# Kernel optimization log

Measured on AMD Instinct MI355X. Metric: run time of the kernel, lower is better.

## Reference

```python
import jax, jax.numpy as jnp
import numpy as np

D_MODEL = 1024
B, S = 4, 4096


def setup_inputs() -> dict:
    key = jax.random.key(0)
    k1, k2, k3, k4, k5 = jax.random.split(key, 5)
    lim = 1.0 / np.sqrt(D_MODEL)  # nn.Linear default init range
    x = jax.random.normal(k1, (B, S, D_MODEL), dtype=jnp.float32)
    mask = jnp.ones((B, S), dtype=jnp.float32)
    W_up = jax.random.uniform(k2, (D_MODEL, D_MODEL), jnp.float32, -lim, lim)
    b_up = jax.random.uniform(k3, (D_MODEL,), jnp.float32, -lim, lim)
    W_f = jax.random.uniform(k4, (D_MODEL, D_MODEL), jnp.float32, -lim, lim)
    b_f = jax.random.uniform(k5, (D_MODEL,), jnp.float32, -lim, lim)
    decay_param = jnp.zeros((1,), dtype=jnp.float32)
    return {"x": x, "mask": mask, "W_up": W_up, "b_up": b_up,
            "W_f": W_f, "b_f": b_f, "decay_param": decay_param}


def _decay_scan(u, decay):
    # h_t = decay * h_{t-1} + u_t  along axis=1, via associative scan.
    # Element: (a, b) representing h -> a*h + b; compose: (a1*a2, b1*a2 + b2).
    a = jnp.broadcast_to(decay, u.shape)

    def combine(c1, c2):
        a1, b1 = c1
        a2, b2 = c2
        return a1 * a2, b1 * a2 + b2

    _, h = jax.lax.associative_scan(combine, (a, u), axis=1)
    return h


def reference(x, mask, W_up, b_up, W_f, b_f, decay_param):
    decay = jax.nn.sigmoid(decay_param)[0]
    # u_i = mask_i * linear_update(x_i)
    u = (jnp.einsum('bsd,ed->bse', x, W_up) + b_up) * mask[..., None]
    # h_t = sum_{i<=t} decay^(t-i) * u_i  (exponential-decay recurrence)
    h = _decay_scan(u, decay)
    return jnp.einsum('bsd,ed->bse', h, W_f) + b_f
```

## Files before the change

kernel.cpp:

```cpp
#include <hip/hip_runtime.h>
#include <hip/hip_bf16.h>
#include <cstdint>
#include <cstddef>

#define DMODEL 1024
#define BATCH  4
#define SEQ    4096
#define BSROWS (BATCH*SEQ)
#define CHUNK  32
#define NCHUNK (SEQ/CHUNK)
#define NCH_T  (BATCH*NCHUNK)

typedef __attribute__((ext_vector_type(8))) short bf16x8;
typedef __attribute__((ext_vector_type(4))) float f32x4;


__device__ __forceinline__ unsigned short f2bf(float f) {
  union { float f; uint32_t u; } v; v.f = f;
  uint32_t u = v.u;
  u += 0x7FFFu + ((u >> 16) & 1u);
  return (unsigned short)(u >> 16);
}

__device__ __forceinline__ float sigmoid_dev(const float* dp) {
  return 1.0f / (1.0f + expf(-dp[0]));
}

typedef __attribute__((address_space(1))) void void_g;
typedef __attribute__((address_space(3))) void void_l;

__device__ __forceinline__ void gl2lds16(const void* g, void* l) {
  __builtin_amdgcn_global_load_lds((void_g*)g, (void_l*)l, 16, 0, 0);
}

__device__ __forceinline__ void kloop64(
    const unsigned short* __restrict__ A, const unsigned short* __restrict__ B,
    int m0, int n0, f32x4 acc[2][2],
    unsigned short* As, unsigned short* Bs, int tid) {
  int lane = tid & 63, w = tid >> 6, wm = w & 1, wn = w >> 1;
  int quad = lane >> 4, l16 = lane & 15;
  int r = tid >> 3, cch = tid & 7;
  int g = cch ^ (r & 7);
  const bf16x8* Av = (const bf16x8*)As;
  const bf16x8* Bv = (const bf16x8*)Bs;
  for (int k0 = 0; k0 < DMODEL; k0 += 64) {
    gl2lds16(A + (size_t)(m0 + r) * DMODEL + k0 + g * 8,      As + r * 64 + cch * 8);
    gl2lds16(A + (size_t)(m0 + 32 + r) * DMODEL + k0 + g * 8, As + (32 + r) * 64 + cch * 8);
    gl2lds16(B + (size_t)(n0 + r) * DMODEL + k0 + g * 8,      Bs + r * 64 + cch * 8);
    gl2lds16(B + (size_t)(n0 + 32 + r) * DMODEL + k0 + g * 8, Bs + (32 + r) * 64 + cch * 8);
    __syncthreads();
    #pragma unroll
    for (int kk = 0; kk < 2; ++kk) {
      bf16x8 af[2], bfr[2];
      #pragma unroll
      for (int i = 0; i < 2; ++i) {
        int rowA = wm * 32 + i * 16 + l16;
        af[i]  = Av[rowA * 8 + ((kk * 4 + quad) ^ (l16 & 7))];
        int rowB = wn * 32 + i * 16 + l16;
        bfr[i] = Bv[rowB * 8 + ((kk * 4 + quad) ^ (l16 & 7))];
      }
      #pragma unroll
      for (int i = 0; i < 2; ++i)
        #pragma unroll
        for (int j = 0; j < 2; ++j)
          acc[i][j] = __builtin_amdgcn_mfma_f32_16x16x32_bf16(af[i], bfr[j], acc[i][j], 0, 0, 0);
    }
    __syncthreads();
  }
}

__global__ __launch_bounds__(256) void prep_kernel(
    const float* __restrict__ x, const float* __restrict__ mask,
    const float* __restrict__ W_up, const float* __restrict__ b_up,
    const float* __restrict__ W_f, const float* __restrict__ dp,
    unsigned short* __restrict__ Wf_bf, unsigned short* __restrict__ WupT,
    float* __restrict__ bb, unsigned short* __restrict__ hv,
    float* __restrict__ carry, float* __restrict__ lbeta,
    float* __restrict__ cbeta) {
  __shared__ float tile[32][33];
  int blk = blockIdx.x;
  int tid = threadIdx.x;

  if (blk < 512) {
    float decay = sigmoid_dev(dp);
    int b = blk / NCHUNK, c = blk % NCHUNK;
    int base = b * SEQ + c * CHUNK;
    const float4* xp = (const float4*)(x + (size_t)base * DMODEL);
    const float4* mp4 = (const float4*)(mask + base);
    float mreg[32];
    #pragma unroll
    for (int q = 0; q < 8; ++q) {
      float4 t = mp4[q];
      mreg[q * 4 + 0] = t.x; mreg[q * 4 + 1] = t.y;
      mreg[q * 4 + 2] = t.z; mreg[q * 4 + 3] = t.w;
    }
    float4 h = make_float4(0.f, 0.f, 0.f, 0.f);
    #pragma unroll
    for (int s = 0; s < CHUNK; ++s) {
      float m = mreg[s];
      float4 xv = xp[(size_t)s * (DMODEL / 4) + tid];
      h.x = decay * h.x + m * xv.x;
      h.y = decay * h.y + m * xv.y;
      h.z = decay * h.z + m * xv.z;
      h.w = decay * h.w + m * xv.w;
      ushort4 o;
      o.x = f2bf(h.x); o.y = f2bf(h.y); o.z = f2bf(h.z); o.w = f2bf(h.w);
      ((ushort4*)hv)[(size_t)(base + s) * (DMODEL / 4) + tid] = o;
    }
    ((float4*)carry)[(size_t)blk * (DMODEL / 4) + tid] = h;
  } else if (blk < 1536) {
    int e = blk - 512;
    int lane = tid & 63, w = tid >> 6;
    float4 v = ((const float4*)(W_f + (size_t)e * DMODEL))[tid];
    float4 bu = ((const float4*)b_up)[tid];
    ushort4 o;
    o.x = f2bf(v.x); o.y = f2bf(v.y); o.z = f2bf(v.z); o.w = f2bf(v.w);
    ((ushort4*)(Wf_bf + (size_t)e * DMODEL))[tid] = o;
    float s = v.x * bu.x + v.y * bu.y + v.z * bu.z + v.w * bu.w;
    #pragma unroll
    for (int off = 32; off; off >>= 1) s += __shfl_down(s, off);
    if (lane == 0) ((float*)tile)[w] = s;
    __syncthreads();
    if (tid == 0)
      bb[e] = ((float*)tile)[0] + ((float*)tile)[1] +
              ((float*)tile)[2] + ((float*)tile)[3];
  } else if (blk < 2560) {
    int id = blk - 1536;
    int bx = id & 31, by = id >> 5;
    int tx = tid & 31, ty = tid >> 5;
    int xx = bx * 32 + tx;
    int y0 = by * 32;
    for (int j = ty; j < 32; j += 8)
      tile[j][tx] = W_up[(size_t)(y0 + j) * DMODEL + xx];
    __syncthreads();
    int ox = by * 32 + tx;
    int oy0 = bx * 32;
    for (int j = ty; j < 32; j += 8)
      WupT[(size_t)(oy0 + j) * DMODEL + ox] = f2bf(tile[tx][j]);
  } else {
    float decay = sigmoid_dev(dp);
    int t = (blk - 2560) * 256 + tid;
    int s = t & 31;
    int cbase = t & ~31;
    float hb = 0.f;
    for (int i = 0; i <= s; ++i)
      hb = decay * hb + mask[cbase + i];
    lbeta[t] = hb;
    if (s == 31) cbeta[t >> 5] = hb;
  }
}

__global__ __launch_bounds__(256) void mid2_kernel(
    const unsigned short* __restrict__ Wf_bf,
    const unsigned short* __restrict__ WupT,
    unsigned short* __restrict__ Wc,
    const float* __restrict__ carry, const float* __restrict__ cbeta,
    const float* __restrict__ dp,
    unsigned short* __restrict__ Pbf, float* __restrict__ pbeta) {
  __shared__ unsigned short As[64 * 64];
  __shared__ unsigned short Bs[64 * 64];
  int tid = threadIdx.x;
  if (blockIdx.x < 256) {
    int mt = blockIdx.x >> 4, nt = blockIdx.x & 15;
    f32x4 acc[2][2] = {};
    kloop64(Wf_bf, WupT, mt * 64, nt * 64, acc, As, Bs, tid);
    int lane = tid & 63, w = tid >> 6, wm = w & 1, wn = w >> 1;
    int quad = lane >> 4, l16 = lane & 15;
    #pragma unroll
    for (int j = 0; j < 2; ++j) {
      int col = nt * 64 + wn * 32 + j * 16 + l16;
      #pragma unroll
      for (int i = 0; i < 2; ++i) {
        int rowb = mt * 64 + wm * 32 + i * 16 + quad * 4;
        #pragma unroll
        for (int rr = 0; rr < 4; ++rr)
          Wc[(size_t)(rowb + rr) * DMODEL + col] = f2bf(acc[i][j][rr]);
      }
    }
  } else {
    float decay = sigmoid_dev(dp);
    float dL = powf(decay, (float)CHUNK);
    int gid = (blockIdx.x - 256) * 256 + tid;
    int b = gid >> 10, dd = gid & 1023;
    float P = 0.f;
    for (int c0 = 0; c0 < NCHUNK; c0 += 8) {
      float v[8];
      #pragma unroll
      for (int j = 0; j < 8; ++j)
        v[j] = carry[(size_t)(b * NCHUNK + c0 + j) * DMODEL + dd];
      #pragma unroll
      for (int j = 0; j < 8; ++j) {
        Pbf[(size_t)(b * NCHUNK + c0 + j) * DMODEL + dd] = f2bf(P);
        P = dL * P + v[j];
      }
    }
    if (dd == 0) {
      float Pb = 0.f;
      for (int c0 = 0; c0 < NCHUNK; c0 += 16) {
        float v[16];
        #pragma unroll
        for (int j = 0; j < 16; ++j) v[j] = cbeta[b * NCHUNK + c0 + j];
        #pragma unroll
        for (int j = 0; j < 16; ++j) {
          pbeta[b * NCHUNK + c0 + j] = Pb;
          Pb = dL * Pb + v[j];
        }
      }
    }
  }
}

__global__ __launch_bounds__(256) void pout_kernel(
    const unsigned short* __restrict__ Pbf,
    const unsigned short* __restrict__ Wc,
    const float* __restrict__ pbeta, const float* __restrict__ bb,
    float* __restrict__ Pout) {
  __shared__ unsigned short As[64 * 64];
  __shared__ unsigned short Bs[64 * 64];
  int tid = threadIdx.x;
  int mt = blockIdx.x >> 4, nt = blockIdx.x & 15;
  f32x4 acc[2][2] = {};
  kloop64(Pbf, Wc, mt * 64, nt * 64, acc, As, Bs, tid);
  int lane = tid & 63, w = tid >> 6, wm = w & 1, wn = w >> 1;
  int quad = lane >> 4, l16 = lane & 15;
  #pragma unroll
  for (int j = 0; j < 2; ++j) {
    int col = nt * 64 + wn * 32 + j * 16 + l16;
    float bbv = bb[col];
    #pragma unroll
    for (int i = 0; i < 2; ++i) {
      int rowb = mt * 64 + wm * 32 + i * 16 + quad * 4;
      #pragma unroll
      for (int rr = 0; rr < 4; ++rr) {
        int row = rowb + rr;
        Pout[(size_t)row * DMODEL + col] = acc[i][j][rr] + pbeta[row] * bbv;
      }
    }
  }
}

__global__ __launch_bounds__(256) void gemm_main(
    const unsigned short* __restrict__ A,
    const unsigned short* __restrict__ Bm,
    const float* __restrict__ Pout,
    const float* __restrict__ lbeta,
    const float* __restrict__ bb,
    const float* __restrict__ bias_f,
    const float* __restrict__ dp,
    float* __restrict__ out) {
  __shared__ unsigned short As[128 * 32];
  __shared__ unsigned short Bs[128 * 32];
  __shared__ float dpow[CHUNK];
  int tid = threadIdx.x;
  if (tid < CHUNK) {
    float decay = sigmoid_dev(dp);
    dpow[tid] = powf(decay, (float)(tid + 1));
  }
  int lane = tid & 63, w = tid >> 6, wm = w & 1, wn = w >> 1;
  int quad = lane >> 4, l16 = lane & 15;
  int r = tid >> 2;
  int c4 = tid & 3;
  int g = c4 ^ ((r >> 1) & 3);
  int phi = (l16 >> 1) & 3;
  int m0 = (blockIdx.x & 127) * 128;
  int n0 = (blockIdx.x >> 7) * 128;
  f32x4 acc[4][4] = {};
  const bf16x8* Av = (const bf16x8*)As;
  const bf16x8* Bv = (const bf16x8*)Bs;
  for (int k0 = 0; k0 < DMODEL; k0 += 32) {
    gl2lds16(A + (size_t)(m0 + r) * DMODEL + k0 + g * 8,        As + r * 32 + c4 * 8);
    gl2lds16(A + (size_t)(m0 + 64 + r) * DMODEL + k0 + g * 8,   As + (64 + r) * 32 + c4 * 8);
    gl2lds16(Bm + (size_t)(n0 + r) * DMODEL + k0 + g * 8,       Bs + r * 32 + c4 * 8);
    gl2lds16(Bm + (size_t)(n0 + 64 + r) * DMODEL + k0 + g * 8,  Bs + (64 + r) * 32 + c4 * 8);
    __syncthreads();
    bf16x8 af[4], bfr[4];
    #pragma unroll
    for (int i = 0; i < 4; ++i) {
      int rowA = wm * 64 + i * 16 + l16;
      af[i]  = Av[rowA * 4 + (quad ^ phi)];
      int rowB = wn * 64 + i * 16 + l16;
      bfr[i] = Bv[rowB * 4 + (quad ^ phi)];
    }
    #pragma unroll
    for (int i = 0; i < 4; ++i)
      #pragma unroll
      for (int j = 0; j < 4; ++j)
        acc[i][j] = __builtin_amdgcn_mfma_f32_16x16x32_bf16(af[i], bfr[j], acc[i][j], 0, 0, 0);
    __syncthreads();
  }
  #pragma unroll
  for (int j = 0; j < 4; ++j) {
    int col = n0 + wn * 64 + j * 16 + l16;
    float bbv = bb[col];
    float bfv = bias_f[col];
    #pragma unroll
    for (int i = 0; i < 4; ++i) {
      int rowb = m0 + wm * 64 + i * 16 + quad * 4;
      #pragma unroll
      for (int rr = 0; rr < 4; ++rr) {
        int row = rowb + rr;
        float po = Pout[(size_t)(row >> 5) * DMODEL + col];
        out[(size_t)row * DMODEL + col] =
            acc[i][j][rr] + dpow[row & 31] * po + lbeta[row] * bbv + bfv;
      }
    }
  }
}


extern "C" void kernel_launch(void* const* d_in, const int* in_sizes, int n_in,
                              void* d_out, int out_size, void* d_ws, size_t ws_size,
                              hipStream_t stream) {
  const float* x    = (const float*)d_in[0];
  const float* mask = (const float*)d_in[1];
  const float* W_up = (const float*)d_in[2];
  const float* b_up = (const float*)d_in[3];
  const float* W_f  = (const float*)d_in[4];
  const float* b_f  = (const float*)d_in[5];
  const float* dp   = (const float*)d_in[6];
  float* out = (float*)d_out;

  char* ws = (char*)d_ws;
  unsigned short* hv    = (unsigned short*)(ws);
  unsigned short* Wc    = (unsigned short*)(ws + 33554432);
  unsigned short* Wf_bf = (unsigned short*)(ws + 35651584);
  unsigned short* WupT  = (unsigned short*)(ws + 37748736);
  float* carry  = (float*)(ws + 39845888);
  unsigned short* Pbf = (unsigned short*)(ws + 41943040);
  float* Pout   = (float*)(ws + 42991616);
  float* lbeta  = (float*)(ws + 45088768);
  float* cbeta  = (float*)(ws + 45154304);
  float* pbeta  = (float*)(ws + 45156352);
  float* bb     = (float*)(ws + 45158400);

  prep_kernel<<<2624, 256, 0, stream>>>(x, mask, W_up, b_up, W_f, dp,
                                        Wf_bf, WupT, bb, hv, carry, lbeta, cbeta);
  mid2_kernel<<<272, 256, 0, stream>>>(Wf_bf, WupT, Wc, carry, cbeta, dp,
                                       Pbf, pbeta);
  pout_kernel<<<128, 256, 0, stream>>>(Pbf, Wc, pbeta, bb, Pout);
  gemm_main<<<1024, 256, 0, stream>>>(hv, Wc, Pout, lbeta, bb, b_f, dp, out);
}
```

Measured before the change: 203.8 us.

## Triple-buffer LDS tiles with async prefetch in all GEMM k-loops

Replaces the single-buffered load/sync/compute loop in kloop64 and gemm_main with a three-slot LDS ring. Each step issues global-to-LDS loads two tiles ahead, waits with vmcnt, and uses one barrier per step. MFMA sections are wrapped in s_setprio, and the gemm_main epilogue is reordered to hoist per-row loads. The goal is to overlap global memory latency with MFMA work, at the cost of three times the LDS footprint, which may lower occupancy.

Result: no change. 201.2 us (-1.3%).

```diff
diff --git a/kernel.cpp b/kernel.cpp
--- a/kernel.cpp
+++ b/kernel.cpp
@@ -41,14 +41,19 @@
   int quad = lane >> 4, l16 = lane & 15;
   int r = tid >> 3, cch = tid & 7;
   int g = cch ^ (r & 7);
-  const bf16x8* Av = (const bf16x8*)As;
-  const bf16x8* Bv = (const bf16x8*)Bs;
-  for (int k0 = 0; k0 < DMODEL; k0 += 64) {
-    gl2lds16(A + (size_t)(m0 + r) * DMODEL + k0 + g * 8,      As + r * 64 + cch * 8);
-    gl2lds16(A + (size_t)(m0 + 32 + r) * DMODEL + k0 + g * 8, As + (32 + r) * 64 + cch * 8);
-    gl2lds16(B + (size_t)(n0 + r) * DMODEL + k0 + g * 8,      Bs + r * 64 + cch * 8);
-    gl2lds16(B + (size_t)(n0 + 32 + r) * DMODEL + k0 + g * 8, Bs + (32 + r) * 64 + cch * 8);
-    __syncthreads();
+
+  auto stage = [&](int t, int slot) {
+    int k0 = t * 64;
+    unsigned short* dA = As + slot * 4096;
+    unsigned short* dB = Bs + slot * 4096;
+    gl2lds16(A + (size_t)(m0 + r) * DMODEL + k0 + g * 8,      dA + r * 64 + cch * 8);
+    gl2lds16(A + (size_t)(m0 + 32 + r) * DMODEL + k0 + g * 8, dA + (32 + r) * 64 + cch * 8);
+    gl2lds16(B + (size_t)(n0 + r) * DMODEL + k0 + g * 8,      dB + r * 64 + cch * 8);
+    gl2lds16(B + (size_t)(n0 + 32 + r) * DMODEL + k0 + g * 8, dB + (32 + r) * 64 + cch * 8);
+  };
+  auto compute = [&](int slot) {
+    const bf16x8* Av = (const bf16x8*)(As + slot * 4096);
+    const bf16x8* Bv = (const bf16x8*)(Bs + slot * 4096);
     #pragma unroll
     for (int kk = 0; kk < 2; ++kk) {
       bf16x8 af[2], bfr[2];
@@ -59,14 +64,36 @@
         int rowB = wn * 32 + i * 16 + l16;
         bfr[i] = Bv[rowB * 8 + ((kk * 4 + quad) ^ (l16 & 7))];
       }
+      __builtin_amdgcn_s_setprio(1);
       #pragma unroll
       for (int i = 0; i < 2; ++i)
         #pragma unroll
         for (int j = 0; j < 2; ++j)
           acc[i][j] = __builtin_amdgcn_mfma_f32_16x16x32_bf16(af[i], bfr[j], acc[i][j], 0, 0, 0);
-    }
-    __syncthreads();
-  }
+      __builtin_amdgcn_s_setprio(0);
+    }
+  };
+
+  stage(0, 0); stage(1, 1);
+  asm volatile("s_waitcnt vmcnt(4)" ::: "memory");
+  __builtin_amdgcn_s_barrier();
+  asm volatile("" ::: "memory");
+  int cur = 0;
+  for (int t = 0; t < 14; ++t) {
+    int ns = cur + 2; if (ns >= 3) ns -= 3;
+    stage(t + 2, ns);
+    compute(cur);
+    asm volatile("s_waitcnt vmcnt(4)" ::: "memory");
+    __builtin_amdgcn_s_barrier();
+    asm volatile("" ::: "memory");
+    cur = (cur == 2) ? 0 : cur + 1;
+  }
+  compute(cur);
+  asm volatile("s_waitcnt vmcnt(0)" ::: "memory");
+  __builtin_amdgcn_s_barrier();
+  asm volatile("" ::: "memory");
+  cur = (cur == 2) ? 0 : cur + 1;
+  compute(cur);
 }
 
 __global__ __launch_bounds__(256) void prep_kernel(
@@ -157,8 +184,8 @@
     const float* __restrict__ carry, const float* __restrict__ cbeta,
     const float* __restrict__ dp,
     unsigned short* __restrict__ Pbf, float* __restrict__ pbeta) {
-  __shared__ unsigned short As[64 * 64];
-  __shared__ unsigned short Bs[64 * 64];
+  __shared__ unsigned short As[3 * 64 * 64];
+  __shared__ unsigned short Bs[3 * 64 * 64];
   int tid = threadIdx.x;
   if (blockIdx.x < 256) {
     int mt = blockIdx.x >> 4, nt = blockIdx.x & 15;
@@ -215,8 +242,8 @@
     const unsigned short* __restrict__ Wc,
     const float* __restrict__ pbeta, const float* __restrict__ bb,
     float* __restrict__ Pout) {
-  __shared__ unsigned short As[64 * 64];
-  __shared__ unsigned short Bs[64 * 64];
+  __shared__ unsigned short As[3 * 64 * 64];
+  __shared__ unsigned short Bs[3 * 64 * 64];
   int tid = threadIdx.x;
   int mt = blockIdx.x >> 4, nt = blockIdx.x & 15;
   f32x4 acc[2][2] = {};
@@ -248,14 +275,15 @@
     const float* __restrict__ bias_f,
     const float* __restrict__ dp,
     float* __restrict__ out) {
-  __shared__ unsigned short As[128 * 32];
-  __shared__ unsigned short Bs[128 * 32];
+  __shared__ unsigned short As[3 * 128 * 32];
+  __shared__ unsigned short Bs[3 * 128 * 32];
   __shared__ float dpow[CHUNK];
   int tid = threadIdx.x;
   if (tid < CHUNK) {
     float decay = sigmoid_dev(dp);
     dpow[tid] = powf(decay, (float)(tid + 1));
   }
+  __syncthreads();
   int lane = tid & 63, w = tid >> 6, wm = w & 1, wn = w >> 1;
   int quad = lane >> 4, l16 = lane & 15;
   int r = tid >> 2;
@@ -265,14 +293,19 @@
   int m0 = (blockIdx.x & 127) * 128;
   int n0 = (blockIdx.x >> 7) * 128;
   f32x4 acc[4][4] = {};
-  const bf16x8* Av = (const bf16x8*)As;
-  const bf16x8* Bv = (const bf16x8*)Bs;
-  for (int k0 = 0; k0 < DMODEL; k0 += 32) {
-    gl2lds16(A + (size_t)(m0 + r) * DMODEL + k0 + g * 8,        As + r * 32 + c4 * 8);
-    gl2lds16(A + (size_t)(m0 + 64 + r) * DMODEL + k0 + g * 8,   As + (64 + r) * 32 + c4 * 8);
-    gl2lds16(Bm + (size_t)(n0 + r) * DMODEL + k0 + g * 8,       Bs + r * 32 + c4 * 8);
-    gl2lds16(Bm + (size_t)(n0 + 64 + r) * DMODEL + k0 + g * 8,  Bs + (64 + r) * 32 + c4 * 8);
-    __syncthreads();
+
+  auto stage = [&](int t, int slot) {
+    int k0 = t * 32;
+    unsigned short* dA = As + slot * (128 * 32);
+    unsigned short* dB = Bs + slot * (128 * 32);
+    gl2lds16(A  + (size_t)(m0 + r) * DMODEL + k0 + g * 8,       dA + r * 32 + c4 * 8);
+    gl2lds16(A  + (size_t)(m0 + 64 + r) * DMODEL + k0 + g * 8,  dA + (64 + r) * 32 + c4 * 8);
+    gl2lds16(Bm + (size_t)(n0 + r) * DMODEL + k0 + g * 8,       dB + r * 32 + c4 * 8);
+    gl2lds16(Bm + (size_t)(n0 + 64 + r) * DMODEL + k0 + g * 8,  dB + (64 + r) * 32 + c4 * 8);
+  };
+  auto compute = [&](int slot) {
+    const bf16x8* Av = (const bf16x8*)(As + slot * (128 * 32));
+    const bf16x8* Bv = (const bf16x8*)(Bs + slot * (128 * 32));
     bf16x8 af[4], bfr[4];
     #pragma unroll
     for (int i = 0; i < 4; ++i) {
@@ -281,27 +314,56 @@
       int rowB = wn * 64 + i * 16 + l16;
       bfr[i] = Bv[rowB * 4 + (quad ^ phi)];
     }
+    __builtin_amdgcn_s_setprio(1);
     #pragma unroll
     for (int i = 0; i < 4; ++i)
       #pragma unroll
       for (int j = 0; j < 4; ++j)
         acc[i][j] = __builtin_amdgcn_mfma_f32_16x16x32_bf16(af[i], bfr[j], acc[i][j], 0, 0, 0);
-    __syncthreads();
-  }
+    __builtin_amdgcn_s_setprio(0);
+  };
+
+  stage(0, 0); stage(1, 1);
+  asm volatile("s_waitcnt vmcnt(4)" ::: "memory");
+  __builtin_amdgcn_s_barrier();
+  asm volatile("" ::: "memory");
+  int cur = 0;
+  for (int t = 0; t < 30; ++t) {
+    int ns = cur + 2; if (ns >= 3) ns -= 3;
+    stage(t + 2, ns);
+    compute(cur);
+    asm volatile("s_waitcnt vmcnt(4)" ::: "memory");
+    __builtin_amdgcn_s_barrier();
+    asm volatile("" ::: "memory");
+    cur = (cur == 2) ? 0 : cur + 1;
+  }
+  compute(cur);
+  asm volatile("s_waitcnt vmcnt(0)" ::: "memory");
+  __builtin_amdgcn_s_barrier();
+  asm volatile("" ::: "memory");
+  cur = (cur == 2) ? 0 : cur + 1;
+  compute(cur);
+
+  float bbv[4], bfv[4];
   #pragma unroll
   for (int j = 0; j < 4; ++j) {
     int col = n0 + wn * 64 + j * 16 + l16;
-    float bbv = bb[col];
-    float bfv = bias_f[col];
-    #pragma unroll
-    for (int i = 0; i < 4; ++i) {
-      int rowb = m0 + wm * 64 + i * 16 + quad * 4;
-      #pragma unroll
-      for (int rr = 0; rr < 4; ++rr) {
-        int row = rowb + rr;
-        float po = Pout[(size_t)(row >> 5) * DMODEL + col];
-        out[(size_t)row * DMODEL + col] =
-            acc[i][j][rr] + dpow[row & 31] * po + lbeta[row] * bbv + bfv;
+    bbv[j] = bb[col];
+    bfv[j] = bias_f[col];
+  }
+  #pragma unroll
+  for (int i = 0; i < 4; ++i) {
+    #pragma unroll
+    for (int rr = 0; rr < 4; ++rr) {
+      int row = m0 + wm * 64 + i * 16 + quad * 4 + rr;
+      float lb  = lbeta[row];
+      float dpw = dpow[row & 31];
+      const float* poRow = Pout + (size_t)(row >> 5) * DMODEL;
+      float* outRow = out + (size_t)row * DMODEL;
+      #pragma unroll
+      for (int j = 0; j < 4; ++j) {
+        int col = n0 + wn * 64 + j * 16 + l16;
+        outRow[col] = acc[i][j][rr] + dpw * poRow[col] + lb * bbv[j] + bfv[j];
       }
     }
   }
```
